# Kernel optimization log

Hardware: AMD Instinct MI355X
Metric: run time of the kernel (lower is better)

Reference implementation:

```python
import jax, jax.numpy as jnp
import numpy as np
from jax import lax

NUM_LABELS = 64  # groundtruth labels in [0, 64); label 0 = background (ignored in pair counts)


def _edges(H, W):
    # channel 0: edge (i,j)-(i+1,j); channel 1: edge (i,j)-(i,j+1)
    idx = np.arange(H * W).reshape(H, W)
    u0 = idx.copy(); v0 = np.roll(idx, -1, axis=0)
    u0[-1, :] = 0; v0[-1, :] = 0  # invalid boundary edges -> self edge, no-op
    u1 = idx.copy(); v1 = np.roll(idx, -1, axis=1)
    u1[:, -1] = 0; v1[:, -1] = 0
    u = np.concatenate([u0.ravel(), u1.ravel()]).astype(np.int32)
    v = np.concatenate([v0.ravel(), v1.ravel()]).astype(np.int32)
    return jnp.asarray(u), jnp.asarray(v)


def _find(parent, x, iters):
    # union-by-size keeps tree depth <= log2(N)+1, so a fixed number of hops suffices
    return lax.fori_loop(0, iters, lambda i, p: parent[p], x)


def _npairs(order, u, v, labels, pos):
    """Kruskal over edges sorted by descending affinity; for each merging edge,
    count pairs of voxels for which it is the maximin edge (pos: same nonzero
    label; neg: different nonzero labels). Pure int computation (non-diff)."""
    N = labels.shape[0]
    iters = int(np.ceil(np.log2(N))) + 2
    parent0 = jnp.arange(N, dtype=jnp.int32)
    size0 = jnp.ones(N, jnp.int32)
    counts0 = jax.nn.one_hot(labels, NUM_LABELS, dtype=jnp.int32)  # [N, L] label histogram per root

    def step(carry, e):
        parent, size, counts = carry
        ru = _find(parent, u[e], iters)
        rv = _find(parent, v[e], iters)
        cu = counts[ru]; cv = counts[rv]
        same = jnp.dot(cu[1:], cv[1:])          # same-nonzero-label pairs
        tu = cu[1:].sum(); tv = cv[1:].sum()    # nonzero-label voxel counts
        n = same if pos else tu * tv - same     # differing-label pairs for neg pass
        merge = ru != rv
        n = jnp.where(merge, n, 0)
        big = jnp.where(size[ru] >= size[rv], ru, rv)
        small = ru + rv - big
        parent = parent.at[small].set(jnp.where(merge, big, parent[small]))
        size = size.at[big].add(jnp.where(merge, size[small], 0))
        counts = counts.at[big].add(jnp.where(merge, counts[small], 0))
        return (parent, size, counts), n

    _, n = lax.scan(step, (parent0, size0, counts0), order)
    return n  # [E] int32, aligned with sorted order


def _malis_grad(aff, labels, u, v):
    # aff [E] float, labels [N] int. MALIS pseudo-loss gradients:
    # pos pass grad_e = n_pos_e * (a_e - 1); neg pass grad_e = n_neg_e * a_e;
    # combined = -(pos + neg) / 2 (as in MalisLoss.forward).
    order = jnp.argsort(-lax.stop_gradient(aff)).astype(jnp.int32)
    a_sorted = aff[order]
    n_pos = _npairs(order, u, v, labels, True).astype(aff.dtype)
    n_neg = _npairs(order, u, v, labels, False).astype(aff.dtype)
    g_sorted = n_pos * (a_sorted - 1.0) + n_neg * a_sorted
    return jnp.zeros_like(aff).at[order].set(-0.5 * g_sorted)


def setup_inputs() -> dict:
    key = jax.random.key(0)
    k1, k2 = jax.random.split(key)
    affinities = jax.random.uniform(k1, (2, 2, 128, 128), dtype=jnp.float32)
    groundtruth = jax.random.randint(k2, (2, 128, 128), 0, NUM_LABELS, dtype=jnp.int64)
    return {"affinities": affinities, "groundtruth": groundtruth}


def reference(affinities, groundtruth):
    B, C, H, W = affinities.shape
    u, v = _edges(H, W)
    aff = affinities.reshape(B, C * H * W)
    lab = groundtruth.reshape(B, H * W).astype(jnp.int32)
    grads = jax.vmap(lambda a, l: _malis_grad(a, l, u, v))(aff, lab)
    return grads.sum()  # pseudo_loss
```

## Files before the change

kernel.cpp:

```cpp
#include <hip/hip_runtime.h>

#define HDIM 128
#define WDIM 128
#define NPIX (HDIM * WDIM)
#define NEDGE (2 * NPIX)
#define BANDS 256
#define MAXK 256

typedef unsigned long long ull;

__device__ __forceinline__ void decode_edge(unsigned e, int& u, int& v) {
  if (e >= (unsigned)NEDGE) { u = 0; v = 0; return; }
  if (e < NPIX) {
    if (e < NPIX - WDIM) { u = (int)e; v = (int)e + WDIM; } else { u = 0; v = 0; }
  } else {
    unsigned t2 = e - NPIX;
    if ((t2 & (WDIM - 1)) != (WDIM - 1)) { u = (int)t2; v = (int)t2 + 1; } else { u = 0; v = 0; }
  }
}

__device__ __forceinline__ int bucket_of(float a) {
  int f = (int)(a * 256.0f);
  f = f < 0 ? 0 : (f > 255 ? 255 : f);
  return 255 - f;
}

__device__ __forceinline__ int cc_find(volatile unsigned* p, int x) {
  int px = (int)p[x];
  while (px != x) {
    int g = (int)p[px];
    if (g != px) p[x] = (unsigned)g;
    x = px; px = g;
  }
  return x;
}

__device__ __forceinline__ void uf_find2(unsigned* pn, int x, int y,
                                         int& rx, int& ry,
                                         unsigned& nzx, unsigned& nzy) {
  unsigned wx = pn[x];
  unsigned wy = pn[y];
  while (true) {
    int px = (int)(wx & 0xFFFFu);
    int py = (int)(wy & 0xFFFFu);
    bool mx = (px != x);
    bool my = (py != y);
    if (!mx && !my) break;
    if (mx) {
      unsigned wpx = pn[px];
      int gx = (int)(wpx & 0xFFFFu);
      if (gx != px) { pn[x] = (wx & 0xFFFF0000u) | (unsigned)gx; x = gx; wx = pn[gx]; }
      else { x = px; wx = wpx; }
    }
    if (my) {
      unsigned wpy = pn[py];
      int gy = (int)(wpy & 0xFFFFu);
      if (gy != py) { pn[y] = (wy & 0xFFFF0000u) | (unsigned)gy; y = gy; wy = pn[gy]; }
      else { y = py; wy = wpy; }
    }
  }
  rx = x; ry = y; nzx = wx >> 16; nzy = wy >> 16;
}

__device__ __forceinline__ ull shflx64(ull x, int m) {
  int lo = __shfl_xor((int)(unsigned)x, m, 64);
  int hi = __shfl_xor((int)(unsigned)(x >> 32), m, 64);
  return ((ull)(unsigned)hi << 32) | (unsigned)lo;
}

__global__ __launch_bounds__(1024) void band_kernel(const int* __restrict__ gt,
                                                    const float* __restrict__ aff_g,
                                                    float* __restrict__ out) {
  __shared__ unsigned pn[NPIX];
  __shared__ ull skbuf[MAXK];
  __shared__ unsigned scnt;
  const int img = blockIdx.x / BANDS;
  const int braw = blockIdx.x % BANDS;
  const int band = (img & 1) ? (BANDS - 1 - braw) : braw;
  const int* lab = gt + (size_t)img * NPIX;
  const float* aff = aff_g + (size_t)img * NEDGE;
  const int tid = threadIdx.x;

  if (band == 0) {
    if (tid < 64) pn[tid] = 0;
    __syncthreads();
    for (int i = tid; i < NPIX; i += 1024) atomicAdd(&pn[(unsigned)lab[i] & 63u], 1u);
    __syncthreads();
    if (tid == 0) {
      double s = 0.0;
      for (int l = 1; l < 64; ++l) { double m = (double)pn[l]; s += m * (m - 1.0) * 0.5; }
      atomicAdd(out, (float)(0.5 * s));
    }
    __syncthreads();
  }

  for (int i = tid; i < NPIX / 4; i += 1024) {
    uint4 w; w.x = 4u * i; w.y = 4u * i + 1u; w.z = 4u * i + 2u; w.w = 4u * i + 3u;
    ((uint4*)pn)[i] = w;
  }
  if (tid == 0) scnt = 0;
  __syncthreads();

  volatile unsigned* vp = pn;
  const float4* aff4 = (const float4*)aff;
  for (int t4 = tid; t4 < NEDGE / 4; t4 += 1024) {
    const float4 q = aff4[t4];
#pragma unroll
    for (int s = 0; s < 4; ++s) {
      const float a = (s == 0) ? q.x : (s == 1) ? q.y : (s == 2) ? q.z : q.w;
      const int b = bucket_of(a);
      if (b > band) continue;
      const unsigned e = (unsigned)(t4 * 4 + s);
      int u, v; decode_edge(e, u, v);
      if (u == v) continue;
      if (b == band) {
        unsigned bits = __float_as_uint(a);
        unsigned ob = (bits & 0x80000000u) ? ~bits : (bits | 0x80000000u);
        unsigned pos = atomicAdd(&scnt, 1u);
        if (pos < MAXK) skbuf[pos] = ((ull)(~ob) << 32) | e;
      } else {
        while (true) {
          int ru = cc_find(vp, u), rv = cc_find(vp, v);
          if (ru == rv) break;
          if (ru < rv) { int t = ru; ru = rv; rv = t; }
          unsigned old = atomicCAS(&pn[ru], (unsigned)ru, (unsigned)rv);
          if (old == (unsigned)ru) break;
          u = ru; v = rv;
        }
      }
    }
  }
  __syncthreads();
  unsigned cnt = scnt; if (cnt > MAXK) cnt = MAXK;

  ull myv[4];
  if (tid < 64) {
    const int lane = tid;
#pragma unroll
    for (int r = 0; r < 4; ++r) {
      unsigned idx = (unsigned)(r * 64 + lane);
      myv[r] = (idx < cnt) ? skbuf[idx] : ~0ull;
    }
#pragma unroll
    for (unsigned k = 2; k <= 256; k <<= 1) {
#pragma unroll
      for (unsigned j = k >> 1; j; j >>= 1) {
        if (j >= 64) {
          const int rj = (int)(j >> 6);
#pragma unroll
          for (int r = 0; r < 4; ++r) {
            if (!(r & rj)) {
              const int p = r | rj;
              const bool dir = ((((unsigned)r << 6) & k) == 0);
              ull a0 = myv[r], a1 = myv[p];
              if ((a0 > a1) == dir) { myv[r] = a1; myv[p] = a0; }
            }
          }
        } else {
#pragma unroll
          for (int r = 0; r < 4; ++r) {
            ull pv = shflx64(myv[r], (int)j);
            const bool low = ((lane & (int)j) == 0);
            const bool dir = (((((unsigned)r << 6) | (unsigned)lane) & k) == 0);
            const bool takemin = (low == dir);
            const bool less = (myv[r] < pv);
            myv[r] = (less == takemin) ? myv[r] : pv;
          }
        }
      }
    }
  } else {
    const int t = tid - 64;
    int prev = -1; unsigned acc = 0; bool multi = false;
    for (int k = 0; k < 18; ++k) {
      int i = t + k * 960;
      if (i >= NPIX) break;
      int r = i; unsigned p;
      while (((p = vp[r]) & 0xFFFFu) != (unsigned)r) r = (int)(p & 0xFFFFu);
      if (i != r) pn[i] = (unsigned)r;
      unsigned c = (lab[i] != 0) ? 1u : 0u;
      if (r != prev) {
        if (prev >= 0) { if (acc) atomicAdd(&pn[prev], acc << 16); multi = true; }
        prev = r; acc = c;
      } else {
        acc += c;
      }
    }
    const int wl = tid & 63;
    int first = __shfl(prev, 0);
    bool uni = __all(!multi && prev == first);
    if (uni) {
      unsigned s = acc;
      for (int off = 32; off; off >>= 1) s += __shfl_down(s, off);
      if (wl == 0 && s) atomicAdd(&pn[prev], s << 16);
    } else if (acc) {
      atomicAdd(&pn[prev], acc << 16);
    }
  }
  __syncthreads();

  if (tid < 64) {
    const int lane = tid;
    double acc = 0.0;
#pragma unroll
    for (int b8 = 0; b8 < 4; ++b8) {
      if ((unsigned)(b8 * 64) >= cnt) break;
      const ull myk_b = myv[b8];
      unsigned e = (unsigned)myk_b;
      unsigned khi = (unsigned)(myk_b >> 32);
      int u, v; decode_edge(e, u, v);
      const bool valid = (u != v);
      unsigned ob = ~khi;
      unsigned bits = (ob & 0x80000000u) ? (ob & 0x7FFFFFFFu) : ~ob;
      const float a = __uint_as_float(bits);

      int ru, rv; unsigned nzu, nzv;
      uf_find2(pn, u, v, ru, rv, nzu, nzv);

      unsigned long long m = __ballot(valid && (ru != rv));
      int myW = 0, myL = 0; unsigned snap = 0;
      while (m) {
        const int j = (int)(__ffsll(m) - 1);
        m &= m - 1;
        const int ruj = __builtin_amdgcn_readlane(ru, j);
        const int rvj = __builtin_amdgcn_readlane(rv, j);
        const unsigned nzuj = (unsigned)__builtin_amdgcn_readlane((int)nzu, j);
        const unsigned nzvj = (unsigned)__builtin_amdgcn_readlane((int)nzv, j);
        const bool live = (ruj != rvj);
        const unsigned mnz = nzuj + nzvj;
        int W = (nzuj >= nzvj) ? ruj : rvj;
        int L = ruj + rvj - W;
        W = live ? W : -1;
        L = live ? L : -1;
        const int sj = live ? j : 64;
        const unsigned spk = nzuj | (nzvj << 16);
        const bool turn = (lane == sj);
        if (turn) { myW = W; myL = L; snap = spk; }
        const bool uW = (ru == W), uL = (ru == L);
        const bool vW = (rv == W), vL = (rv == L);
        if (uL) ru = W;
        if (uW | uL) nzu = mnz;
        if (vL) rv = W;
        if (vW | vL) nzv = mnz;
      }
      pn[u] = (unsigned)ru;
      pn[v] = (unsigned)rv;
      if (myW != myL) {
        pn[myL] = (unsigned)myW;
        acc += (double)((snap & 0xFFFFu) * (snap >> 16)) * (double)a;
      }
      pn[ru] = (nzu << 16) | (unsigned)ru;
      pn[rv] = (nzv << 16) | (unsigned)rv;
    }
    for (int off = 32; off > 0; off >>= 1) acc += __shfl_down(acc, off);
    if (lane == 0) atomicAdd(out, (float)(-0.5 * acc));
  }
}

extern "C" void kernel_launch(void* const* d_in, const int* in_sizes, int n_in,
                              void* d_out, int out_size, void* d_ws, size_t ws_size,
                              hipStream_t stream) {
  const float* aff = (const float*)d_in[0];
  const int* gt = (const int*)d_in[1];
  float* out = (float*)d_out;
  const int B = in_sizes[1] / NPIX;

  hipMemsetAsync(d_out, 0, sizeof(float) * (size_t)out_size, stream);
  band_kernel<<<dim3(B * BANDS), dim3(1024), 0, stream>>>(gt, aff, out);
}
```

Before: 131.7 us.

## Precompute union-find checkpoints every 32 bands to shorten per-band prefix merging

Adds a pre-pass kernel that builds global union-find forests for seven checkpoints, each covering all edges with bucket below a multiple of 32, using atomic CAS linking in the workspace. Each band block then loads the nearest checkpoint forest into shared memory and unions only the edges between the checkpoint and its band, rather than all higher-affinity edges. This cuts the redundant prefix connectivity work repeated across 256 bands. The cost is an extra memset, an extra kernel launch, and a 16K-entry global read per block.

```diff
diff --git a/kernel.cpp b/kernel.cpp
--- a/kernel.cpp
+++ b/kernel.cpp
@@ -6,6 +6,9 @@
 #define NEDGE (2 * NPIX)
 #define BANDS 256
 #define MAXK 256
+#define NCP 7
+#define CPSL 32
+#define SENT 0xFFFFFFFFu
 
 typedef unsigned long long ull;
 
@@ -23,6 +26,47 @@
   int f = (int)(a * 256.0f);
   f = f < 0 ? 0 : (f > 255 ? 255 : f);
   return 255 - f;
+}
+
+__device__ __forceinline__ unsigned gld(const unsigned* p) {
+  return __hip_atomic_load(p, __ATOMIC_RELAXED, __HIP_MEMORY_SCOPE_AGENT);
+}
+__device__ __forceinline__ void gst(unsigned* p, unsigned v) {
+  __hip_atomic_store(p, v, __ATOMIC_RELAXED, __HIP_MEMORY_SCOPE_AGENT);
+}
+__device__ __forceinline__ int gfind(unsigned* p, int x) {
+  while (true) {
+    unsigned px = gld(&p[x]);
+    if (px == SENT) return x;
+    unsigned gp = gld(&p[(int)px]);
+    if (gp == SENT) return (int)px;
+    gst(&p[x], gp);
+    x = (int)gp;
+  }
+}
+
+__global__ __launch_bounds__(1024) void cp_kernel(const float* __restrict__ aff_g,
+                                                  unsigned* __restrict__ parents) {
+  const int bid = blockIdx.x;
+  const int img = bid / (NCP * CPSL);
+  const int r = bid % (NCP * CPSL);
+  const int c = r / CPSL + 1;
+  const int s = r % CPSL;
+  const float* aff = aff_g + (size_t)img * NEDGE;
+  unsigned* par = parents + ((size_t)img * NCP + (c - 1)) * NPIX;
+  const int e = s * (NEDGE / CPSL) + threadIdx.x;
+  const float a = aff[e];
+  if (bucket_of(a) >= c * 32) return;
+  int u, v; decode_edge((unsigned)e, u, v);
+  if (u == v) return;
+  while (true) {
+    int ru = gfind(par, u), rv = gfind(par, v);
+    if (ru == rv) return;
+    if (ru < rv) { int t = ru; ru = rv; rv = t; }
+    unsigned old = atomicCAS(&par[ru], SENT, (unsigned)rv);
+    if (old == SENT) return;
+    u = ru; v = rv;
+  }
 }
 
 __device__ __forceinline__ int cc_find(volatile unsigned* p, int x) {
@@ -70,6 +114,7 @@
 
 __global__ __launch_bounds__(1024) void band_kernel(const int* __restrict__ gt,
                                                     const float* __restrict__ aff_g,
+                                                    const unsigned* __restrict__ parents,
                                                     float* __restrict__ out) {
   __shared__ unsigned pn[NPIX];
   __shared__ ull skbuf[MAXK];
@@ -94,9 +139,23 @@
     __syncthreads();
   }
 
-  for (int i = tid; i < NPIX / 4; i += 1024) {
-    uint4 w; w.x = 4u * i; w.y = 4u * i + 1u; w.z = 4u * i + 2u; w.w = 4u * i + 3u;
-    ((uint4*)pn)[i] = w;
+  const int cbase = band & ~31;
+  if (cbase == 0) {
+    for (int i = tid; i < NPIX / 4; i += 1024) {
+      uint4 w; w.x = 4u * i; w.y = 4u * i + 1u; w.z = 4u * i + 2u; w.w = 4u * i + 3u;
+      ((uint4*)pn)[i] = w;
+    }
+  } else {
+    const unsigned* par = parents + ((size_t)img * NCP + (band >> 5) - 1) * NPIX;
+    for (int i = tid; i < NPIX / 4; i += 1024) {
+      uint4 w = ((const uint4*)par)[i];
+      const unsigned b0 = 4u * (unsigned)i;
+      w.x = (w.x == SENT) ? b0 : w.x;
+      w.y = (w.y == SENT) ? b0 + 1u : w.y;
+      w.z = (w.z == SENT) ? b0 + 2u : w.z;
+      w.w = (w.w == SENT) ? b0 + 3u : w.w;
+      ((uint4*)pn)[i] = w;
+    }
   }
   if (tid == 0) scnt = 0;
   __syncthreads();
@@ -109,7 +168,7 @@
     for (int s = 0; s < 4; ++s) {
       const float a = (s == 0) ? q.x : (s == 1) ? q.y : (s == 2) ? q.z : q.w;
       const int b = bucket_of(a);
-      if (b > band) continue;
+      if (b > band || b < cbase) continue;
       const unsigned e = (unsigned)(t4 * 4 + s);
       int u, v; decode_edge(e, u, v);
       if (u == v) continue;
@@ -264,7 +323,10 @@
   const int* gt = (const int*)d_in[1];
   float* out = (float*)d_out;
   const int B = in_sizes[1] / NPIX;
+  unsigned* parents = (unsigned*)d_ws;
 
   hipMemsetAsync(d_out, 0, sizeof(float) * (size_t)out_size, stream);
-  band_kernel<<<dim3(B * BANDS), dim3(1024), 0, stream>>>(gt, aff, out);
-}
+  hipMemsetAsync(d_ws, 0xFF, (size_t)B * NCP * NPIX * sizeof(unsigned), stream);
+  cp_kernel<<<dim3(B * NCP * CPSL), dim3(1024), 0, stream>>>(aff, parents);
+  band_kernel<<<dim3(B * BANDS), dim3(1024), 0, stream>>>(gt, aff, parents, out);
+}
```

Result: slower. 192.8 us (+46.4%).

## Split band kernel into parallel compression pass and small-wavefront sort/merge pass

Applied to the files above, without the earlier changes.

The single kernel, where one wavefront sorted and merged band edges while 960 threads sat idle, is split in two. The first kernel builds the connected components and maps each band edge's endpoint roots to compact component IDs through a shared-memory hash table. It writes keys, compact IDs and per-component nonzero counts to workspace. A second 64-thread kernel does the bitonic sort and serial Kruskal merge over a 512-entry parent array, freeing the big blocks sooner at the cost of an extra launch and a global-memory round-trip.

```diff
diff --git a/kernel.cpp b/kernel.cpp
--- a/kernel.cpp
+++ b/kernel.cpp
@@ -6,6 +6,8 @@
 #define NEDGE (2 * NPIX)
 #define BANDS 256
 #define MAXK 256
+#define NCID 512
+#define HTSZ 1024
 
 typedef unsigned long long ull;
 
@@ -68,18 +70,44 @@
   return ((ull)(unsigned)hi << 32) | (unsigned)lo;
 }
 
-__global__ __launch_bounds__(1024) void band_kernel(const int* __restrict__ gt,
-                                                    const float* __restrict__ aff_g,
-                                                    float* __restrict__ out) {
+__device__ __forceinline__ unsigned cid_of(unsigned root, unsigned* htab, unsigned* hcnt) {
+  unsigned h = (root * 2654435761u) >> 22;
+  const unsigned tag = (root + 1u) << 16;
+  while (true) {
+    unsigned cur = htab[h & (HTSZ - 1)];
+    if (cur == 0u) {
+      unsigned cid = atomicAdd(hcnt, 1u);
+      unsigned old = atomicCAS(&htab[h & (HTSZ - 1)], 0u, tag | cid);
+      if (old == 0u) return cid;
+      cur = old;
+    }
+    if ((cur & 0xFFFF0000u) == tag) return cur & 0xFFFFu;
+    ++h;
+  }
+}
+
+__global__ __launch_bounds__(1024) void band_a(const int* __restrict__ gt,
+                                               const float* __restrict__ aff_g,
+                                               ull* __restrict__ keys_g,
+                                               unsigned* __restrict__ cids_g,
+                                               unsigned* __restrict__ nzt_g,
+                                               unsigned* __restrict__ cnt_g,
+                                               float* __restrict__ out) {
   __shared__ unsigned pn[NPIX];
   __shared__ ull skbuf[MAXK];
-  __shared__ unsigned scnt;
+  __shared__ unsigned htab[HTSZ];
+  __shared__ unsigned nzt[NCID];
+  __shared__ unsigned scnt, ccnt;
   const int img = blockIdx.x / BANDS;
   const int braw = blockIdx.x % BANDS;
   const int band = (img & 1) ? (BANDS - 1 - braw) : braw;
   const int* lab = gt + (size_t)img * NPIX;
   const float* aff = aff_g + (size_t)img * NEDGE;
   const int tid = threadIdx.x;
+
+  if (tid < HTSZ) htab[tid] = 0u;
+  if (tid < NCID) nzt[tid] = 0u;
+  if (tid == 0) { scnt = 0u; ccnt = 0u; }
 
   if (band == 0) {
     if (tid < 64) pn[tid] = 0;
@@ -98,7 +126,6 @@
     uint4 w; w.x = 4u * i; w.y = 4u * i + 1u; w.z = 4u * i + 2u; w.w = 4u * i + 3u;
     ((uint4*)pn)[i] = w;
   }
-  if (tid == 0) scnt = 0;
   __syncthreads();
 
   volatile unsigned* vp = pn;
@@ -133,43 +160,7 @@
   __syncthreads();
   unsigned cnt = scnt; if (cnt > MAXK) cnt = MAXK;
 
-  ull myv[4];
-  if (tid < 64) {
-    const int lane = tid;
-#pragma unroll
-    for (int r = 0; r < 4; ++r) {
-      unsigned idx = (unsigned)(r * 64 + lane);
-      myv[r] = (idx < cnt) ? skbuf[idx] : ~0ull;
-    }
-#pragma unroll
-    for (unsigned k = 2; k <= 256; k <<= 1) {
-#pragma unroll
-      for (unsigned j = k >> 1; j; j >>= 1) {
-        if (j >= 64) {
-          const int rj = (int)(j >> 6);
-#pragma unroll
-          for (int r = 0; r < 4; ++r) {
-            if (!(r & rj)) {
-              const int p = r | rj;
-              const bool dir = ((((unsigned)r << 6) & k) == 0);
-              ull a0 = myv[r], a1 = myv[p];
-              if ((a0 > a1) == dir) { myv[r] = a1; myv[p] = a0; }
-            }
-          }
-        } else {
-#pragma unroll
-          for (int r = 0; r < 4; ++r) {
-            ull pv = shflx64(myv[r], (int)j);
-            const bool low = ((lane & (int)j) == 0);
-            const bool dir = (((((unsigned)r << 6) | (unsigned)lane) & k) == 0);
-            const bool takemin = (low == dir);
-            const bool less = (myv[r] < pv);
-            myv[r] = (less == takemin) ? myv[r] : pv;
-          }
-        }
-      }
-    }
-  } else {
+  if (tid >= 64) {
     const int t = tid - 64;
     int prev = -1; unsigned acc = 0; bool multi = false;
     for (int k = 0; k < 18; ++k) {
@@ -199,62 +190,143 @@
   }
   __syncthreads();
 
-  if (tid < 64) {
-    const int lane = tid;
-    double acc = 0.0;
-#pragma unroll
-    for (int b8 = 0; b8 < 4; ++b8) {
-      if ((unsigned)(b8 * 64) >= cnt) break;
-      const ull myk_b = myv[b8];
-      unsigned e = (unsigned)myk_b;
-      unsigned khi = (unsigned)(myk_b >> 32);
-      int u, v; decode_edge(e, u, v);
-      const bool valid = (u != v);
-      unsigned ob = ~khi;
-      unsigned bits = (ob & 0x80000000u) ? (ob & 0x7FFFFFFFu) : ~ob;
-      const float a = __uint_as_float(bits);
-
-      int ru, rv; unsigned nzu, nzv;
-      uf_find2(pn, u, v, ru, rv, nzu, nzv);
-
-      unsigned long long m = __ballot(valid && (ru != rv));
-      int myW = 0, myL = 0; unsigned snap = 0;
-      while (m) {
-        const int j = (int)(__ffsll(m) - 1);
-        m &= m - 1;
-        const int ruj = __builtin_amdgcn_readlane(ru, j);
-        const int rvj = __builtin_amdgcn_readlane(rv, j);
-        const unsigned nzuj = (unsigned)__builtin_amdgcn_readlane((int)nzu, j);
-        const unsigned nzvj = (unsigned)__builtin_amdgcn_readlane((int)nzv, j);
-        const bool live = (ruj != rvj);
-        const unsigned mnz = nzuj + nzvj;
-        int W = (nzuj >= nzvj) ? ruj : rvj;
-        int L = ruj + rvj - W;
-        W = live ? W : -1;
-        L = live ? L : -1;
-        const int sj = live ? j : 64;
-        const unsigned spk = nzuj | (nzvj << 16);
-        const bool turn = (lane == sj);
-        if (turn) { myW = W; myL = L; snap = spk; }
-        const bool uW = (ru == W), uL = (ru == L);
-        const bool vW = (rv == W), vL = (rv == L);
-        if (uL) ru = W;
-        if (uW | uL) nzu = mnz;
-        if (vL) rv = W;
-        if (vW | vL) nzv = mnz;
+  if (tid < (int)cnt) {
+    const ull key = skbuf[tid];
+    const unsigned e = (unsigned)key;
+    int u, v; decode_edge(e, u, v);
+    const unsigned ru = pn[u] & 0xFFFFu;
+    const unsigned rv = pn[v] & 0xFFFFu;
+    const unsigned cu = cid_of(ru, htab, &ccnt);
+    const unsigned cv = cid_of(rv, htab, &ccnt);
+    nzt[cu] = pn[ru] >> 16;
+    nzt[cv] = pn[rv] >> 16;
+    keys_g[(size_t)blockIdx.x * MAXK + tid] =
+        (key & 0xFFFFFFFF00000000ull) | ((ull)(e << 16)) | (unsigned)tid;
+    cids_g[(size_t)blockIdx.x * MAXK + tid] = (cu << 16) | cv;
+  }
+  __syncthreads();
+  if (tid < NCID) nzt_g[(size_t)blockIdx.x * NCID + tid] = nzt[tid];
+  if (tid == 0) cnt_g[blockIdx.x] = cnt;
+}
+
+__global__ __launch_bounds__(64) void band_b(const ull* __restrict__ keys_g,
+                                             const unsigned* __restrict__ cids_g,
+                                             const unsigned* __restrict__ nzt_g,
+                                             const unsigned* __restrict__ cnt_g,
+                                             float* __restrict__ out) {
+  __shared__ unsigned pn2[NCID];
+  __shared__ unsigned cid2[MAXK];
+  const int bid = blockIdx.x;
+  const int lane = threadIdx.x;
+  const unsigned cnt = cnt_g[bid];
+
+#pragma unroll
+  for (int r = 0; r < NCID / 64; ++r) {
+    const int i = r * 64 + lane;
+    pn2[i] = (nzt_g[(size_t)bid * NCID + i] << 16) | (unsigned)i;
+  }
+#pragma unroll
+  for (int r = 0; r < MAXK / 64; ++r) {
+    const int j = r * 64 + lane;
+    cid2[j] = cids_g[(size_t)bid * MAXK + j];
+  }
+  ull myv[4];
+#pragma unroll
+  for (int r = 0; r < 4; ++r) {
+    const unsigned idx = (unsigned)(r * 64 + lane);
+    myv[r] = (idx < cnt) ? keys_g[(size_t)bid * MAXK + idx] : ~0ull;
+  }
+  __syncthreads();
+
+#pragma unroll
+  for (unsigned k = 2; k <= 256; k <<= 1) {
+#pragma unroll
+    for (unsigned j = k >> 1; j; j >>= 1) {
+      if (j >= 64) {
+        const int rj = (int)(j >> 6);
+#pragma unroll
+        for (int r = 0; r < 4; ++r) {
+          if (!(r & rj)) {
+            const int p = r | rj;
+            const bool dir = ((((unsigned)r << 6) & k) == 0);
+            ull a0 = myv[r], a1 = myv[p];
+            if ((a0 > a1) == dir) { myv[r] = a1; myv[p] = a0; }
+          }
+        }
+      } else {
+#pragma unroll
+        for (int r = 0; r < 4; ++r) {
+          ull pv = shflx64(myv[r], (int)j);
+          const bool low = ((lane & (int)j) == 0);
+          const bool dir = (((((unsigned)r << 6) | (unsigned)lane) & k) == 0);
+          const bool takemin = (low == dir);
+          const bool less = (myv[r] < pv);
+          myv[r] = (less == takemin) ? myv[r] : pv;
+        }
       }
-      pn[u] = (unsigned)ru;
-      pn[v] = (unsigned)rv;
-      if (myW != myL) {
-        pn[myL] = (unsigned)myW;
-        acc += (double)((snap & 0xFFFFu) * (snap >> 16)) * (double)a;
-      }
-      pn[ru] = (nzu << 16) | (unsigned)ru;
-      pn[rv] = (nzv << 16) | (unsigned)rv;
-    }
-    for (int off = 32; off > 0; off >>= 1) acc += __shfl_down(acc, off);
-    if (lane == 0) atomicAdd(out, (float)(-0.5 * acc));
-  }
+    }
+  }
+
+  unsigned cp_[4];
+#pragma unroll
+  for (int r = 0; r < 4; ++r) {
+    const unsigned pos = (unsigned)myv[r] & 0xFFu;
+    cp_[r] = (myv[r] != ~0ull) ? cid2[pos] : 0u;
+  }
+
+  double acc = 0.0;
+#pragma unroll
+  for (int b8 = 0; b8 < 4; ++b8) {
+    if ((unsigned)(b8 * 64) >= cnt) break;
+    const ull myk_b = myv[b8];
+    const bool valid = (myk_b != ~0ull);
+    const int u = (int)(cp_[b8] >> 16);
+    const int v = (int)(cp_[b8] & 0xFFFFu);
+    const unsigned khi = (unsigned)(myk_b >> 32);
+    const unsigned ob = ~khi;
+    const unsigned bits = (ob & 0x80000000u) ? (ob & 0x7FFFFFFFu) : ~ob;
+    const float a = __uint_as_float(bits);
+
+    int ru, rv; unsigned nzu, nzv;
+    uf_find2(pn2, u, v, ru, rv, nzu, nzv);
+
+    unsigned long long m = __ballot(valid && (ru != rv));
+    int myW = 0, myL = 0; unsigned snap = 0;
+    while (m) {
+      const int j = (int)(__ffsll(m) - 1);
+      m &= m - 1;
+      const int ruj = __builtin_amdgcn_readlane(ru, j);
+      const int rvj = __builtin_amdgcn_readlane(rv, j);
+      const unsigned nzuj = (unsigned)__builtin_amdgcn_readlane((int)nzu, j);
+      const unsigned nzvj = (unsigned)__builtin_amdgcn_readlane((int)nzv, j);
+      const bool live = (ruj != rvj);
+      const unsigned mnz = nzuj + nzvj;
+      int W = (nzuj >= nzvj) ? ruj : rvj;
+      int L = ruj + rvj - W;
+      W = live ? W : -1;
+      L = live ? L : -1;
+      const int sj = live ? j : 64;
+      const unsigned spk = nzuj | (nzvj << 16);
+      const bool turn = (lane == sj);
+      if (turn) { myW = W; myL = L; snap = spk; }
+      const bool uW = (ru == W), uL = (ru == L);
+      const bool vW = (rv == W), vL = (rv == L);
+      if (uL) ru = W;
+      if (uW | uL) nzu = mnz;
+      if (vL) rv = W;
+      if (vW | vL) nzv = mnz;
+    }
+    pn2[u] = (unsigned)ru;
+    pn2[v] = (unsigned)rv;
+    if (myW != myL) {
+      pn2[myL] = (unsigned)myW;
+      acc += (double)((snap & 0xFFFFu) * (snap >> 16)) * (double)a;
+    }
+    pn2[ru] = (nzu << 16) | (unsigned)ru;
+    pn2[rv] = (nzv << 16) | (unsigned)rv;
+  }
+  for (int off = 32; off > 0; off >>= 1) acc += __shfl_down(acc, off);
+  if (lane == 0) atomicAdd(out, (float)(-0.5 * acc));
 }
 
 extern "C" void kernel_launch(void* const* d_in, const int* in_sizes, int n_in,
@@ -264,7 +336,14 @@
   const int* gt = (const int*)d_in[1];
   float* out = (float*)d_out;
   const int B = in_sizes[1] / NPIX;
+  const int NWG = B * BANDS;
+
+  ull* keys = (ull*)d_ws;
+  unsigned* cids = (unsigned*)(keys + (size_t)NWG * MAXK);
+  unsigned* nzt = cids + (size_t)NWG * MAXK;
+  unsigned* cntg = nzt + (size_t)NWG * NCID;
 
   hipMemsetAsync(d_out, 0, sizeof(float) * (size_t)out_size, stream);
-  band_kernel<<<dim3(B * BANDS), dim3(1024), 0, stream>>>(gt, aff, out);
-}
+  band_a<<<dim3(NWG), dim3(1024), 0, stream>>>(gt, aff, keys, cids, nzt, cntg, out);
+  band_b<<<dim3(NWG), dim3(64), 0, stream>>>(keys, cids, nzt, cntg, out);
+}
```

Result: slower. 144.0 us (+9.3%).

## Batch union-find hooks per thread and flatten parents with parallel pointer jumping

Applied to the files above, without the earlier changes.

Each thread now gathers its up-to-four edges that are strictly above the band into packed pairs and then hooks them in wave-uniform loops, instead of running a divergent CAS loop inline for every edge. The float-to-bucket conversion is replaced by direct comparisons against precomputed band thresholds. After hooking, a block-wide pointer-jumping loop using syncthreads_count fully flattens the parent array, so the later counting pass reads roots directly instead of chasing chains. This targets warp divergence and long find chains, at the cost of extra full-array sweeps and block barriers.

```diff
diff --git a/kernel.cpp b/kernel.cpp
--- a/kernel.cpp
+++ b/kernel.cpp
@@ -6,6 +6,7 @@
 #define NEDGE (2 * NPIX)
 #define BANDS 256
 #define MAXK 256
+#define INVP 0xFFFFFFFFu
 
 typedef unsigned long long ull;
 
@@ -17,12 +18,6 @@
     unsigned t2 = e - NPIX;
     if ((t2 & (WDIM - 1)) != (WDIM - 1)) { u = (int)t2; v = (int)t2 + 1; } else { u = 0; v = 0; }
   }
-}
-
-__device__ __forceinline__ int bucket_of(float a) {
-  int f = (int)(a * 256.0f);
-  f = f < 0 ? 0 : (f > 255 ? 255 : f);
-  return 255 - f;
 }
 
 __device__ __forceinline__ int cc_find(volatile unsigned* p, int x) {
@@ -68,6 +63,25 @@
   return ((ull)(unsigned)hi << 32) | (unsigned)lo;
 }
 
+__device__ __forceinline__ void cc_hook_dense(volatile unsigned* vp, unsigned* pn,
+                                              unsigned pk) {
+  bool act = (pk != INVP);
+  if (!__any(act)) return;
+  int u = (int)(pk >> 16), v = (int)(pk & 0xFFFFu);
+  while (__any(act)) {
+    if (act) {
+      int ru = cc_find(vp, u), rv = cc_find(vp, v);
+      if (ru == rv) { act = false; }
+      else {
+        if (ru < rv) { int t = ru; ru = rv; rv = t; }
+        unsigned old = atomicCAS(&pn[ru], (unsigned)ru, (unsigned)rv);
+        if (old == (unsigned)ru) act = false;
+        else { u = ru; v = rv; }
+      }
+    }
+  }
+}
+
 __global__ __launch_bounds__(1024) void band_kernel(const int* __restrict__ gt,
                                                     const float* __restrict__ aff_g,
                                                     float* __restrict__ out) {
@@ -81,6 +95,9 @@
   const float* aff = aff_g + (size_t)img * NEDGE;
   const int tid = threadIdx.x;
 
+  const float lo = (float)(255 - band) * 0.00390625f;
+  const float hi = (float)(256 - band) * 0.00390625f;
+
   if (band == 0) {
     if (tid < 64) pn[tid] = 0;
     __syncthreads();
@@ -105,33 +122,42 @@
   const float4* aff4 = (const float4*)aff;
   for (int t4 = tid; t4 < NEDGE / 4; t4 += 1024) {
     const float4 q = aff4[t4];
+    unsigned p0 = INVP, p1 = INVP, p2 = INVP, p3 = INVP;
 #pragma unroll
     for (int s = 0; s < 4; ++s) {
       const float a = (s == 0) ? q.x : (s == 1) ? q.y : (s == 2) ? q.z : q.w;
-      const int b = bucket_of(a);
-      if (b > band) continue;
+      if (a < lo) continue;
       const unsigned e = (unsigned)(t4 * 4 + s);
       int u, v; decode_edge(e, u, v);
       if (u == v) continue;
-      if (b == band) {
+      if (a < hi) {
         unsigned bits = __float_as_uint(a);
         unsigned ob = (bits & 0x80000000u) ? ~bits : (bits | 0x80000000u);
         unsigned pos = atomicAdd(&scnt, 1u);
         if (pos < MAXK) skbuf[pos] = ((ull)(~ob) << 32) | e;
       } else {
-        while (true) {
-          int ru = cc_find(vp, u), rv = cc_find(vp, v);
-          if (ru == rv) break;
-          if (ru < rv) { int t = ru; ru = rv; rv = t; }
-          unsigned old = atomicCAS(&pn[ru], (unsigned)ru, (unsigned)rv);
-          if (old == (unsigned)ru) break;
-          u = ru; v = rv;
-        }
-      }
-    }
+        p3 = p2; p2 = p1; p1 = p0; p0 = ((unsigned)u << 16) | (unsigned)v;
+      }
+    }
+    cc_hook_dense(vp, pn, p0);
+    cc_hook_dense(vp, pn, p1);
+    cc_hook_dense(vp, pn, p2);
+    cc_hook_dense(vp, pn, p3);
   }
   __syncthreads();
   unsigned cnt = scnt; if (cnt > MAXK) cnt = MAXK;
+
+  while (true) {
+    int changed = 0;
+    for (int i = tid; i < NPIX; i += 1024) {
+      unsigned r = pn[i] & 0xFFFFu;
+      if (r != (unsigned)i) {
+        unsigned g = pn[r] & 0xFFFFu;
+        if (g != r) { pn[i] = g; changed = 1; }
+      }
+    }
+    if (__syncthreads_count(changed) == 0) break;
+  }
 
   ull myv[4];
   if (tid < 64) {
@@ -175,9 +201,7 @@
     for (int k = 0; k < 18; ++k) {
       int i = t + k * 960;
       if (i >= NPIX) break;
-      int r = i; unsigned p;
-      while (((p = vp[r]) & 0xFFFFu) != (unsigned)r) r = (int)(p & 0xFFFFu);
-      if (i != r) pn[i] = (unsigned)r;
+      int r = (int)(pn[i] & 0xFFFFu);
       unsigned c = (lab[i] != 0) ? 1u : 0u;
       if (r != prev) {
         if (prev >= 0) { if (acc) atomicAdd(&pn[prev], acc << 16); multi = true; }
```

Result: slower. 144.7 us (+9.8%).
